# Kernel tuning notes

Hardware: AMD Instinct MI355X
Metric: run time of the kernel (lower is better)

The kernel has to match this reference:

```python
import jax, jax.numpy as jnp
import numpy as np

NUM_GRAPHS = 128
NODES_PER_GRAPH = 512
LATENT_DIM = 256


def setup_inputs() -> dict:
    key = jax.random.key(0)
    n_total = NUM_GRAPHS * NODES_PER_GRAPH
    z = jax.random.normal(key, (n_total, LATENT_DIM), dtype=jnp.float32)
    # sorted graph assignment: nodes of graph i are contiguous
    batch = (jnp.arange(n_total, dtype=jnp.int32) // NODES_PER_GRAPH).astype(jnp.int32)
    return {"z": z, "batch": batch, "num_graphs": NUM_GRAPHS, "max_nodes": NODES_PER_GRAPH}


def reference(z, batch, num_graphs, max_nodes):
    # Eval-mode forward (dropout is identity when not training).
    n_total, d = z.shape
    ones = jnp.ones((n_total,), dtype=jnp.int32)
    counts = jax.ops.segment_sum(ones, batch, num_segments=num_graphs)  # [G]
    starts = jnp.concatenate([jnp.zeros((1,), jnp.int32), jnp.cumsum(counts)[:-1].astype(jnp.int32)])
    pos = jnp.arange(n_total, dtype=jnp.int32) - starts[batch]  # intra-graph node index
    # Scatter nodes into zero-padded [G, max_nodes, D] tensor
    z_pad = jnp.zeros((num_graphs, max_nodes, d), dtype=z.dtype).at[batch, pos].set(z)
    valid = jnp.zeros((num_graphs, max_nodes), dtype=bool).at[batch, pos].set(True)
    # Per-graph inner-product decoder + sigmoid, padded positions forced to 0
    adj = jax.nn.sigmoid(jnp.einsum('gnd,gmd->gnm', z_pad, z_pad))  # [G, N, N]
    mask = valid[:, :, None] & valid[:, None, :]
    return jnp.where(mask, adj, jnp.zeros((), dtype=adj.dtype))
```

## Files before the change

### kernel.cpp

```cpp
#include <hip/hip_runtime.h>

typedef __fp16 fp16x2 __attribute__((ext_vector_type(2)));
typedef _Float16 half8 __attribute__((ext_vector_type(8)));
typedef float floatx4 __attribute__((ext_vector_type(4)));

namespace {

constexpr int NODES = 512;
constexpr int DIM   = 256;
constexpr int BM    = 128;
constexpr int BK    = 64;
constexpr int LSTR  = 72;

union Cvt8 { fp16x2 h2[4]; half8 h8; };

__device__ inline half8 pack8(const float4 f0, const float4 f1) {
  Cvt8 c;
  c.h2[0] = __builtin_amdgcn_cvt_pkrtz(f0.x, f0.y);
  c.h2[1] = __builtin_amdgcn_cvt_pkrtz(f0.z, f0.w);
  c.h2[2] = __builtin_amdgcn_cvt_pkrtz(f1.x, f1.y);
  c.h2[3] = __builtin_amdgcn_cvt_pkrtz(f1.z, f1.w);
  return c.h8;
}

__global__ __launch_bounds__(256, 4)
void decoder_kernel(const float* __restrict__ z, float* __restrict__ out) {
  __shared__ _Float16 As[BM * LSTR];
  __shared__ _Float16 Bs[BM * LSTR];

  const int bid = blockIdx.x;
  const int g    = (bid & 7) + 8 * (bid >> 7);
  const int tile = (bid >> 3) & 15;
  const int tn   = tile >> 2;
  const int tm   = tile & 3;

  const int tid  = threadIdx.x;
  const int lane = tid & 63;
  const int wave = tid >> 6;
  const int wRow = wave >> 1;
  const int wCol = wave & 1;
  const int lrow = lane & 15;
  const int quad = lane >> 4;

  const float* zA = z + ((size_t)g * NODES + tn * BM) * DIM;
  const float* zB = z + ((size_t)g * NODES + tm * BM) * DIM;

  const int srow  = tid >> 1;
  const int shalf = tid & 1;

  floatx4 acc[4][4];
#pragma unroll
  for (int i = 0; i < 4; ++i)
#pragma unroll
    for (int j = 0; j < 4; ++j)
      acc[i][j] = (floatx4){0.f, 0.f, 0.f, 0.f};

  for (int kk = 0; kk < DIM; kk += BK) {
    {
      const float4* pa = reinterpret_cast<const float4*>(zA + srow * DIM + kk + shalf * 32);
      _Float16* da = &As[srow * LSTR + shalf * 32];
      float4 f0 = pa[0], f1 = pa[1], f2 = pa[2], f3 = pa[3];
      *reinterpret_cast<half8*>(da)     = pack8(f0, f1);
      *reinterpret_cast<half8*>(da + 8) = pack8(f2, f3);
      f0 = pa[4]; f1 = pa[5]; f2 = pa[6]; f3 = pa[7];
      *reinterpret_cast<half8*>(da + 16) = pack8(f0, f1);
      *reinterpret_cast<half8*>(da + 24) = pack8(f2, f3);
    }
    {
      const float4* pb = reinterpret_cast<const float4*>(zB + srow * DIM + kk + shalf * 32);
      _Float16* db = &Bs[srow * LSTR + shalf * 32];
      float4 f0 = pb[0], f1 = pb[1], f2 = pb[2], f3 = pb[3];
      *reinterpret_cast<half8*>(db)     = pack8(f0, f1);
      *reinterpret_cast<half8*>(db + 8) = pack8(f2, f3);
      f0 = pb[4]; f1 = pb[5]; f2 = pb[6]; f3 = pb[7];
      *reinterpret_cast<half8*>(db + 16) = pack8(f0, f1);
      *reinterpret_cast<half8*>(db + 24) = pack8(f2, f3);
    }
    __syncthreads();

#pragma unroll
    for (int ks = 0; ks < 2; ++ks) {
      half8 af[4], bf[4];
#pragma unroll
      for (int i = 0; i < 4; ++i)
        af[i] = *reinterpret_cast<const half8*>(
            &As[(wRow * 64 + i * 16 + lrow) * LSTR + ks * 32 + quad * 8]);
#pragma unroll
      for (int j = 0; j < 4; ++j)
        bf[j] = *reinterpret_cast<const half8*>(
            &Bs[(wCol * 64 + j * 16 + lrow) * LSTR + ks * 32 + quad * 8]);

#pragma unroll
      for (int i = 0; i < 4; ++i)
#pragma unroll
        for (int j = 0; j < 4; ++j)
          acc[i][j] = __builtin_amdgcn_mfma_f32_16x16x32_f16(af[i], bf[j], acc[i][j], 0, 0, 0);
    }
    __syncthreads();
  }

  float* outg = out + (size_t)g * NODES * NODES;
  const int nBase = tn * BM + wRow * 64;
  const int mBase = tm * BM + wCol * 64;
#pragma unroll
  for (int i = 0; i < 4; ++i) {
#pragma unroll
    for (int j = 0; j < 4; ++j) {
      const int m = mBase + j * 16 + lrow;
#pragma unroll
      for (int r = 0; r < 4; ++r) {
        const int n = nBase + i * 16 + quad * 4 + r;
        const float x = acc[i][j][r];
        outg[(size_t)n * NODES + m] = __builtin_amdgcn_rcpf(1.0f + __expf(-x));
      }
    }
  }
}

}

extern "C" void kernel_launch(void* const* d_in, const int* in_sizes, int n_in,
                              void* d_out, int out_size, void* d_ws, size_t ws_size,
                              hipStream_t stream) {
  const float* z = (const float*)d_in[0];
  float* out = (float*)d_out;
  dim3 grid(128 * 16);
  dim3 block(256);
  hipLaunchKernelGGL(decoder_kernel, grid, block, 0, stream, z, out);
}
```

Baseline: 233.8 us.

## Pre-convert z to fp16 and stream tiles with async global-to-LDS loads

A separate kernel converts z to fp16 in workspace once, so the GEMM kernel no longer re-reads fp32 and converts for every tile. The GEMM then loads fp16 tiles straight into LDS with global_load_lds, using an XOR swizzle instead of padding to avoid bank conflicts. The cost is an extra launch plus a 32 MB write and read of the fp16 copy. The old fused kernel is kept as a fallback for when the workspace is too small.

```diff
diff --git a/kernel.cpp b/kernel.cpp
--- a/kernel.cpp
+++ b/kernel.cpp
@@ -10,7 +10,6 @@
 constexpr int DIM   = 256;
 constexpr int BM    = 128;
 constexpr int BK    = 64;
-constexpr int LSTR  = 72;
 
 union Cvt8 { fp16x2 h2[4]; half8 h8; };
 
@@ -23,10 +22,25 @@
   return c.h8;
 }
 
+__device__ inline void async_ld16(const void* g, void* lds) {
+  __builtin_amdgcn_global_load_lds(
+      (const __attribute__((address_space(1))) unsigned int*)g,
+      (__attribute__((address_space(3))) unsigned int*)lds,
+      16, 0, 0);
+}
+
+__global__ __launch_bounds__(256)
+void cvt_kernel(const float* __restrict__ z, _Float16* __restrict__ z16) {
+  const int i = blockIdx.x * 256 + threadIdx.x;
+  const float4* p = reinterpret_cast<const float4*>(z) + (size_t)i * 2;
+  const float4 f0 = p[0], f1 = p[1];
+  reinterpret_cast<half8*>(z16)[i] = pack8(f0, f1);
+}
+
 __global__ __launch_bounds__(256, 4)
-void decoder_kernel(const float* __restrict__ z, float* __restrict__ out) {
-  __shared__ _Float16 As[BM * LSTR];
-  __shared__ _Float16 Bs[BM * LSTR];
+void gemm_kernel(const _Float16* __restrict__ z16, float* __restrict__ out) {
+  __shared__ __align__(16) _Float16 As[BM * BK];
+  __shared__ __align__(16) _Float16 Bs[BM * BK];
 
   const int bid = blockIdx.x;
   const int g    = (bid & 7) + 8 * (bid >> 7);
@@ -42,19 +56,100 @@
   const int lrow = lane & 15;
   const int quad = lane >> 4;
 
+  const _Float16* zA = z16 + ((size_t)g * NODES + tn * BM) * DIM;
+  const _Float16* zB = z16 + ((size_t)g * NODES + tm * BM) * DIM;
+
+  const int sRow = lane >> 3;
+  const int sCp  = (lane & 7) ^ sRow;
+  const size_t sOffH = (size_t)sRow * DIM + sCp * 8;
+
+  floatx4 acc[4][4];
+#pragma unroll
+  for (int i = 0; i < 4; ++i)
+#pragma unroll
+    for (int j = 0; j < 4; ++j)
+      acc[i][j] = (floatx4){0.f, 0.f, 0.f, 0.f};
+
+  for (int kk = 0; kk < DIM; kk += BK) {
+#pragma unroll
+    for (int it = 0; it < 4; ++it) {
+      const int q = wave * 4 + it;
+      const _Float16* gA = zA + (size_t)q * 8 * DIM + kk + sOffH;
+      const _Float16* gB = zB + (size_t)q * 8 * DIM + kk + sOffH;
+      async_ld16(gA, &As[q * 512]);
+      async_ld16(gB, &Bs[q * 512]);
+    }
+    __syncthreads();
+
+#pragma unroll
+    for (int ks = 0; ks < 2; ++ks) {
+      half8 af[4], bf[4];
+#pragma unroll
+      for (int i = 0; i < 4; ++i) {
+        const int row = wRow * 64 + i * 16 + lrow;
+        const int cp = (ks * 4 + quad) ^ (lrow & 7);
+        af[i] = *reinterpret_cast<const half8*>(&As[row * BK + cp * 8]);
+      }
+#pragma unroll
+      for (int j = 0; j < 4; ++j) {
+        const int row = wCol * 64 + j * 16 + lrow;
+        const int cp = (ks * 4 + quad) ^ (lrow & 7);
+        bf[j] = *reinterpret_cast<const half8*>(&Bs[row * BK + cp * 8]);
+      }
+#pragma unroll
+      for (int i = 0; i < 4; ++i)
+#pragma unroll
+        for (int j = 0; j < 4; ++j)
+          acc[i][j] = __builtin_amdgcn_mfma_f32_16x16x32_f16(af[i], bf[j], acc[i][j], 0, 0, 0);
+    }
+    __syncthreads();
+  }
+
+  float* outg = out + (size_t)g * NODES * NODES;
+  const int nBase = tn * BM + wRow * 64;
+  const int mBase = tm * BM + wCol * 64;
+#pragma unroll
+  for (int i = 0; i < 4; ++i) {
+#pragma unroll
+    for (int j = 0; j < 4; ++j) {
+      const int m = mBase + j * 16 + lrow;
+#pragma unroll
+      for (int r = 0; r < 4; ++r) {
+        const int n = nBase + i * 16 + quad * 4 + r;
+        const float x = acc[i][j][r];
+        outg[(size_t)n * NODES + m] = __builtin_amdgcn_rcpf(1.0f + __expf(-x));
+      }
+    }
+  }
+}
+
+constexpr int LSTR = 72;
+__global__ __launch_bounds__(256, 4)
+void fallback_kernel(const float* __restrict__ z, float* __restrict__ out) {
+  __shared__ _Float16 As[BM * LSTR];
+  __shared__ _Float16 Bs[BM * LSTR];
+  const int bid = blockIdx.x;
+  const int g    = (bid & 7) + 8 * (bid >> 7);
+  const int tile = (bid >> 3) & 15;
+  const int tn   = tile >> 2;
+  const int tm   = tile & 3;
+  const int tid  = threadIdx.x;
+  const int lane = tid & 63;
+  const int wave = tid >> 6;
+  const int wRow = wave >> 1;
+  const int wCol = wave & 1;
+  const int lrow = lane & 15;
+  const int quad = lane >> 4;
   const float* zA = z + ((size_t)g * NODES + tn * BM) * DIM;
   const float* zB = z + ((size_t)g * NODES + tm * BM) * DIM;
-
   const int srow  = tid >> 1;
   const int shalf = tid & 1;
-
   floatx4 acc[4][4];
 #pragma unroll
   for (int i = 0; i < 4; ++i)
 #pragma unroll
     for (int j = 0; j < 4; ++j)
       acc[i][j] = (floatx4){0.f, 0.f, 0.f, 0.f};
-
   for (int kk = 0; kk < DIM; kk += BK) {
     {
       const float4* pa = reinterpret_cast<const float4*>(zA + srow * DIM + kk + shalf * 32);
@@ -77,7 +172,6 @@
       *reinterpret_cast<half8*>(db + 24) = pack8(f2, f3);
     }
     __syncthreads();
-
 #pragma unroll
     for (int ks = 0; ks < 2; ++ks) {
       half8 af[4], bf[4];
@@ -89,7 +183,6 @@
       for (int j = 0; j < 4; ++j)
         bf[j] = *reinterpret_cast<const half8*>(
             &Bs[(wCol * 64 + j * 16 + lrow) * LSTR + ks * 32 + quad * 8]);
-
 #pragma unroll
       for (int i = 0; i < 4; ++i)
 #pragma unroll
@@ -98,7 +191,6 @@
     }
     __syncthreads();
   }
-
   float* outg = out + (size_t)g * NODES * NODES;
   const int nBase = tn * BM + wRow * 64;
   const int mBase = tm * BM + wCol * 64;
@@ -124,7 +216,12 @@
                               hipStream_t stream) {
   const float* z = (const float*)d_in[0];
   float* out = (float*)d_out;
-  dim3 grid(128 * 16);
-  dim3 block(256);
-  hipLaunchKernelGGL(decoder_kernel, grid, block, 0, stream, z, out);
-}
+  const size_t need = (size_t)128 * 512 * 256 * sizeof(_Float16);
+  if (ws_size >= need) {
+    _Float16* z16 = (_Float16*)d_ws;
+    hipLaunchKernelGGL(cvt_kernel, dim3(8192), dim3(256), 0, stream, z, z16);
+    hipLaunchKernelGGL(gemm_kernel, dim3(128 * 16), dim3(256), 0, stream, z16, out);
+  } else {
+    hipLaunchKernelGGL(fallback_kernel, dim3(128 * 16), dim3(256), 0, stream, z, out);
+  }
+}
```

After: 217.3 us. 7.1% less time.

## Exploit Gram-matrix symmetry: compute upper-triangle tiles, mirror writes, async LDS loads

Applied to the files above, without the earlier changes.

The grid shrinks from 16 tiles per graph to the 10 upper-triangular tiles. Each off-diagonal tile writes both its block and the transposed block, and diagonal tiles reuse the A buffer for B. Global-to-LDS staging now uses direct async loads of fp32 with an XOR swizzle, and the fp16 conversion moves to LDS read time with BK reduced to 32. This is meant to cut redundant MFMA work and input traffic. The cost is strided, scalar transposed stores, an uneven workload between diagonal and off-diagonal blocks, and more syncs per K step.

```diff
diff --git a/kernel.cpp b/kernel.cpp
--- a/kernel.cpp
+++ b/kernel.cpp
@@ -9,8 +9,7 @@
 constexpr int NODES = 512;
 constexpr int DIM   = 256;
 constexpr int BM    = 128;
-constexpr int BK    = 64;
-constexpr int LSTR  = 72;
+constexpr int BK    = 32;
 
 union Cvt8 { fp16x2 h2[4]; half8 h8; };
 
@@ -23,16 +22,26 @@
   return c.h8;
 }
 
+__device__ inline void async_ld16(const void* g, void* lds) {
+  __builtin_amdgcn_global_load_lds(
+      (const __attribute__((address_space(1))) unsigned int*)g,
+      (__attribute__((address_space(3))) unsigned int*)lds,
+      16, 0, 0);
+}
+
 __global__ __launch_bounds__(256, 4)
 void decoder_kernel(const float* __restrict__ z, float* __restrict__ out) {
-  __shared__ _Float16 As[BM * LSTR];
-  __shared__ _Float16 Bs[BM * LSTR];
+  __shared__ __align__(16) float As[BM * BK];
+  __shared__ __align__(16) float Bs[BM * BK];
 
   const int bid = blockIdx.x;
-  const int g    = (bid & 7) + 8 * (bid >> 7);
-  const int tile = (bid >> 3) & 15;
-  const int tn   = tile >> 2;
-  const int tm   = tile & 3;
+  const int idx = bid >> 3;
+  const int gg  = idx / 10;
+  const int t   = idx - gg * 10;
+  const int g   = (bid & 7) + 8 * gg;
+  const int tn  = (int)((0x3221110000ull >> (4 * t)) & 0xF);
+  const int tm  = (int)((0x3323213210ull >> (4 * t)) & 0xF);
+  const bool diag = (tn == tm);
 
   const int tid  = threadIdx.x;
   const int lane = tid & 63;
@@ -45,8 +54,9 @@
   const float* zA = z + ((size_t)g * NODES + tn * BM) * DIM;
   const float* zB = z + ((size_t)g * NODES + tm * BM) * DIM;
 
-  const int srow  = tid >> 1;
-  const int shalf = tid & 1;
+  const int rowl = lane >> 3;
+  const int csw  = (lane & 7) ^ rowl;
+  const size_t sOff = (size_t)rowl * DIM + csw * 4;
 
   floatx4 acc[4][4];
 #pragma unroll
@@ -55,63 +65,64 @@
     for (int j = 0; j < 4; ++j)
       acc[i][j] = (floatx4){0.f, 0.f, 0.f, 0.f};
 
+  const float4* As4 = reinterpret_cast<const float4*>(As);
+  const float4* Bs4 = diag ? As4 : reinterpret_cast<const float4*>(Bs);
+  const int c0 = (2 * quad) ^ (lrow & 7);
+  const int c1 = (2 * quad + 1) ^ (lrow & 7);
+
   for (int kk = 0; kk < DIM; kk += BK) {
-    {
-      const float4* pa = reinterpret_cast<const float4*>(zA + srow * DIM + kk + shalf * 32);
-      _Float16* da = &As[srow * LSTR + shalf * 32];
-      float4 f0 = pa[0], f1 = pa[1], f2 = pa[2], f3 = pa[3];
-      *reinterpret_cast<half8*>(da)     = pack8(f0, f1);
-      *reinterpret_cast<half8*>(da + 8) = pack8(f2, f3);
-      f0 = pa[4]; f1 = pa[5]; f2 = pa[6]; f3 = pa[7];
-      *reinterpret_cast<half8*>(da + 16) = pack8(f0, f1);
-      *reinterpret_cast<half8*>(da + 24) = pack8(f2, f3);
-    }
-    {
-      const float4* pb = reinterpret_cast<const float4*>(zB + srow * DIM + kk + shalf * 32);
-      _Float16* db = &Bs[srow * LSTR + shalf * 32];
-      float4 f0 = pb[0], f1 = pb[1], f2 = pb[2], f3 = pb[3];
-      *reinterpret_cast<half8*>(db)     = pack8(f0, f1);
-      *reinterpret_cast<half8*>(db + 8) = pack8(f2, f3);
-      f0 = pb[4]; f1 = pb[5]; f2 = pb[6]; f3 = pb[7];
-      *reinterpret_cast<half8*>(db + 16) = pack8(f0, f1);
-      *reinterpret_cast<half8*>(db + 24) = pack8(f2, f3);
+#pragma unroll
+    for (int it = 0; it < 4; ++it) {
+      const int q = wave * 4 + it;
+      async_ld16(zA + (size_t)q * 8 * DIM + kk + sOff, &As[q * 256]);
+      if (!diag)
+        async_ld16(zB + (size_t)q * 8 * DIM + kk + sOff, &Bs[q * 256]);
     }
     __syncthreads();
 
+    half8 af[4], bf[4];
 #pragma unroll
-    for (int ks = 0; ks < 2; ++ks) {
-      half8 af[4], bf[4];
+    for (int i = 0; i < 4; ++i) {
+      const int r = wRow * 64 + i * 16 + lrow;
+      const float4 lo = As4[r * 8 + c0];
+      const float4 hi = As4[r * 8 + c1];
+      af[i] = pack8(lo, hi);
+    }
 #pragma unroll
-      for (int i = 0; i < 4; ++i)
-        af[i] = *reinterpret_cast<const half8*>(
-            &As[(wRow * 64 + i * 16 + lrow) * LSTR + ks * 32 + quad * 8]);
+    for (int j = 0; j < 4; ++j) {
+      const int r = wCol * 64 + j * 16 + lrow;
+      const float4 lo = Bs4[r * 8 + c0];
+      const float4 hi = Bs4[r * 8 + c1];
+      bf[j] = pack8(lo, hi);
+    }
+#pragma unroll
+    for (int i = 0; i < 4; ++i)
 #pragma unroll
       for (int j = 0; j < 4; ++j)
-        bf[j] = *reinterpret_cast<const half8*>(
-            &Bs[(wCol * 64 + j * 16 + lrow) * LSTR + ks * 32 + quad * 8]);
-
-#pragma unroll
-      for (int i = 0; i < 4; ++i)
-#pragma unroll
-        for (int j = 0; j < 4; ++j)
-          acc[i][j] = __builtin_amdgcn_mfma_f32_16x16x32_f16(af[i], bf[j], acc[i][j], 0, 0, 0);
-    }
+        acc[i][j] = __builtin_amdgcn_mfma_f32_16x16x32_f16(af[i], bf[j], acc[i][j], 0, 0, 0);
     __syncthreads();
   }
 
   float* outg = out + (size_t)g * NODES * NODES;
-  const int nBase = tn * BM + wRow * 64;
-  const int mBase = tm * BM + wCol * 64;
+  const int nB = tn * BM + wRow * 64;
+  const int mB = tm * BM + wCol * 64;
 #pragma unroll
   for (int i = 0; i < 4; ++i) {
 #pragma unroll
     for (int j = 0; j < 4; ++j) {
-      const int m = mBase + j * 16 + lrow;
-#pragma unroll
-      for (int r = 0; r < 4; ++r) {
-        const int n = nBase + i * 16 + quad * 4 + r;
-        const float x = acc[i][j][r];
-        outg[(size_t)n * NODES + m] = __builtin_amdgcn_rcpf(1.0f + __expf(-x));
+      const int m  = mB + j * 16 + lrow;
+      const int n0 = nB + i * 16 + quad * 4;
+      float4 v;
+      v.x = __builtin_amdgcn_rcpf(1.0f + __expf(-acc[i][j][0]));
+      v.y = __builtin_amdgcn_rcpf(1.0f + __expf(-acc[i][j][1]));
+      v.z = __builtin_amdgcn_rcpf(1.0f + __expf(-acc[i][j][2]));
+      v.w = __builtin_amdgcn_rcpf(1.0f + __expf(-acc[i][j][3]));
+      *reinterpret_cast<float4*>(&outg[(size_t)m * NODES + n0]) = v;
+      if (!diag) {
+        outg[(size_t)(n0 + 0) * NODES + m] = v.x;
+        outg[(size_t)(n0 + 1) * NODES + m] = v.y;
+        outg[(size_t)(n0 + 2) * NODES + m] = v.z;
+        outg[(size_t)(n0 + 3) * NODES + m] = v.w;
       }
     }
   }
@@ -124,7 +135,7 @@
                               hipStream_t stream) {
   const float* z = (const float*)d_in[0];
   float* out = (float*)d_out;
-  dim3 grid(128 * 16);
+  dim3 grid(128 * 10);
   dim3 block(256);
   hipLaunchKernelGGL(decoder_kernel, grid, block, 0, stream, z, out);
 }
```

After: 219.2 us. 1.07x faster.
